# Kernel optimization log

Measured on AMD Instinct MI355X. Metric: run time of the kernel, lower is better.

The kernel has to match this reference:

```python
import jax, jax.numpy as jnp
import numpy as np

EPS = 1e-5      # BatchNorm1d default eps
K = 4           # branching factor of the ontology tree
HID = 6         # num_hiddens_genotype
LEVEL_SIZES = (64, 16, 4, 1)   # leaves -> root (term_layer_list order)
OFFSETS = (0, 64, 80, 84)      # slices into the stacked [85,...] term params


def setup_inputs() -> dict:
    key = jax.random.key(0)
    ks = jax.random.split(key, 8)
    B, G, GD, NT, NL = 4096, 4096, 24, 85, 64
    f32 = jnp.float32
    return {
        "x": jax.random.normal(ks[0], (B, G), f32),
        "gene_W": jax.random.normal(ks[1], (NL, GD, G), f32) * (1.0 / np.sqrt(G)),
        "gene_b": jnp.zeros((NL, GD), f32),
        "term_W": jax.random.normal(ks[2], (NT, HID, GD), f32) * (1.0 / np.sqrt(GD)),
        "term_b": jnp.zeros((NT, HID), f32),
        "bn_gamma": jnp.ones((NT, HID), f32),
        "bn_beta": jnp.zeros((NT, HID), f32),
        "aux1_W": jax.random.normal(ks[3], (NT, 1, HID), f32) * 0.1,
        "aux1_b": jnp.zeros((NT, 1), f32),
        "aux2_W": jax.random.normal(ks[4], (NT, 1, 1), f32) * 0.1,
        "aux2_b": jnp.zeros((NT, 1), f32),
        "final_W": jax.random.normal(ks[5], (HID, HID), f32) * (1.0 / np.sqrt(HID)),
        "final_b": jnp.zeros((HID,), f32),
        "fbn_gamma": jnp.ones((HID,), f32),
        "fbn_beta": jnp.zeros((HID,), f32),
        "faux_W": jax.random.normal(ks[6], (1, HID), f32) * 0.1,
        "faux_b": jnp.zeros((1,), f32),
        "fout_W": jax.random.normal(ks[7], (1, 1), f32) * 0.1,
        "fout_b": jnp.zeros((1,), f32),
    }


def _bn(z, g, b):
    # training-mode BatchNorm1d: batch mean / biased variance over axis 0
    mu = jnp.mean(z, axis=0, keepdims=True)
    var = jnp.mean((z - mu) ** 2, axis=0, keepdims=True)
    return (z - mu) * jax.lax.rsqrt(var + EPS) * g + b


def _forward(x, gene_W, gene_b, term_W, term_b, bn_gamma, bn_beta,
             aux1_W, aux1_b, aux2_W, aux2_b, final_W, final_b,
             fbn_gamma, fbn_beta, faux_W, faux_b, fout_W, fout_b):
    B = x.shape[0]
    # direct_gene_layers for all 64 leaf terms, batched: [B, 64, 24]
    h_in = jnp.einsum('bg,tkg->btk', x, gene_W) + gene_b
    aux_outs = []
    h = None
    for n, o in zip(LEVEL_SIZES, OFFSETS):  # leaves -> root (DAG topo order)
        if h is not None:
            # concat the K=4 children hidden states of each term: [B,n,K*HID]
            h_in = h.reshape(B, n, K * HID)
        # per-term Linear + tanh + BatchNorm, batched over the n terms
        z = jnp.tanh(jnp.einsum('bti,thi->bth', h_in, term_W[o:o + n]) + term_b[o:o + n])
        h = _bn(z, bn_gamma[o:o + n], bn_beta[o:o + n])  # [B, n, HID]
        # aux head: Linear(HID->1) -> tanh -> Linear(1->1)
        a1 = jnp.tanh(jnp.einsum('bth,toh->bto', h, aux1_W[o:o + n]) + aux1_b[o:o + n])
        a2 = a1 * aux2_W[o:o + n, 0] + aux2_b[o:o + n]   # [B, n, 1]
        aux_outs.append(a2[..., 0])
    root = h[:, 0, :]                                    # [B, HID]
    f = jnp.tanh(root @ final_W.T + final_b)
    mu = jnp.mean(f, axis=0)
    var = jnp.mean((f - mu) ** 2, axis=0)
    f = (f - mu) * jax.lax.rsqrt(var + EPS) * fbn_gamma + fbn_beta
    fa = jnp.tanh(f @ faux_W.T + faux_b)                 # [B, 1]
    pred = jax.nn.sigmoid(fa * fout_W[0, 0] + fout_b)    # [B, 1]
    # aux_out_map flattened in topo order, with 'final' prediction last: [B, 86]
    return jnp.concatenate(aux_outs + [pred], axis=1)


def reference(x, gene_W, gene_b, term_W, term_b, bn_gamma, bn_beta,
              aux1_W, aux1_b, aux2_W, aux2_b, final_W, final_b,
              fbn_gamma, fbn_beta, faux_W, faux_b, fout_W, fout_b):
    return _forward(x, gene_W, gene_b, term_W, term_b, bn_gamma, bn_beta,
                    aux1_W, aux1_b, aux2_W, aux2_b, final_W, final_b,
                    fbn_gamma, fbn_beta, faux_W, faux_b, fout_W, fout_b)
```

## Files before the change

### kernel.cpp

```cpp
#include <hip/hip_runtime.h>
#include <stdint.h>
#include <math.h>

#define EPSV   1e-5f
#define BATCH  4096
#define GDIM   4096
#define NF0    384
#define NSPLIT 8

typedef __attribute__((ext_vector_type(8))) short bf16x8;
typedef __attribute__((ext_vector_type(4))) float f32x4;
typedef __attribute__((ext_vector_type(2))) float f32x2;
typedef __attribute__((ext_vector_type(4))) uint32_t u32x4;

__device__ __forceinline__ uint32_t pkbf(float x, float y) {
    uint32_t a = __float_as_uint(x) + 0x8000u;
    uint32_t b = __float_as_uint(y) + 0x8000u;
    return __builtin_amdgcn_perm(b, a, 0x07060302u);
}
__device__ __forceinline__ uint16_t f2bf(float f) {
    return (uint16_t)((__float_as_uint(f) + 0x8000u) >> 16);
}
__device__ __forceinline__ float blo(uint32_t v) {
    union { uint32_t u; float f; } x; x.u = v << 16; return x.f;
}
__device__ __forceinline__ float bhi(uint32_t v) {
    union { uint32_t u; float f; } x; x.u = v & 0xffff0000u; return x.f;
}
__device__ __forceinline__ void glds16(const uint16_t* g, short* l) {
    __builtin_amdgcn_global_load_lds(
        (const __attribute__((address_space(1))) void*)g,
        (__attribute__((address_space(3))) void*)l, 16, 0, 0);
}

__global__ __launch_bounds__(256) void prep_kernel(
    const float* __restrict__ gene_W,
    const float* __restrict__ term_W, const float* __restrict__ term_b,
    const float* __restrict__ gene_b,
    uint16_t* __restrict__ m0, float* __restrict__ stats)
{
    const int tid = threadIdx.x;
    if (blockIdx.x == 0) {
        for (int j = tid; j < 1040; j += 256) stats[j] = 0.f;
        for (int f = tid; f < NF0; f += 256) {
            const int t = f / 6, h = f - t * 6;
            float b = term_b[f];
#pragma unroll
            for (int i = 0; i < 24; ++i)
                b += term_W[t * 144 + h * 24 + i] * gene_b[t * 24 + i];
            stats[1040 + f] = b;
        }
    }
    __shared__ float Wl[144];
    const int bid = blockIdx.x;
    const int t = bid >> 4;
    const int g = ((bid & 15) << 8) + tid;
    if (tid < 144) Wl[tid] = term_W[t * 144 + tid];
    __syncthreads();
    float gw[24];
#pragma unroll
    for (int i = 0; i < 24; ++i)
        gw[i] = gene_W[((size_t)t * 24 + i) * GDIM + g];
#pragma unroll
    for (int h = 0; h < 6; ++h) {
        float s = 0.f;
#pragma unroll
        for (int i = 0; i < 24; ++i) s += Wl[h * 24 + i] * gw[i];
        m0[((size_t)(t * 6 + h)) * GDIM + g] = f2bf(s);
    }
}

__global__ __launch_bounds__(512) void gemm_wide(
    const float* __restrict__ A32, const uint16_t* __restrict__ Bw,
    uint16_t* __restrict__ P, int KC)
{
    const int N = NF0, K = GDIM;
    __shared__ short sA[128 * 64];
    __shared__ short sB[2][384 * 64];
    const int tid  = threadIdx.x;
    const int m0   = blockIdx.x * 128;
    const int kbase = blockIdx.y * KC;
    uint16_t* Cp = P + (size_t)blockIdx.y * ((size_t)BATCH * NF0);
    const int wave = tid >> 6, lane = tid & 63;
    const int wm   = (wave >> 2) * 64;
    const int wn   = (wave & 3) * 96;
// ... 49 lines not shown
            for (int n = 0; n < 6; ++n)
                bfr[n] = *(const bf16x8*)&sB[cur][(wn + n * 16 + lm) * 64 + kk * 32 + quad * 8];
#pragma unroll
            for (int m = 0; m < 4; ++m)
#pragma unroll
                for (int n = 0; n < 6; ++n)
                    acc[m][n] = __builtin_amdgcn_mfma_f32_16x16x32_bf16(
                        af[m], bfr[n], acc[m][n], 0, 0, 0);
        }
        __builtin_amdgcn_s_barrier();
        a0 = n0v; a1 = n1v; a2 = n2v; a3 = n3v;
        cur ^= 1;
    }
    asm volatile("s_waitcnt vmcnt(0)" ::: "memory");
    {
        u32x4 pa0 = (u32x4){pkbf(a0[0],a0[1]), pkbf(a0[2],a0[3]),
                            pkbf(a1[0],a1[1]), pkbf(a1[2],a1[3])};
        u32x4 pa1 = (u32x4){pkbf(a2[0],a2[1]), pkbf(a2[2],a2[3]),
                            pkbf(a3[0],a3[1]), pkbf(a3[2],a3[3])};
        *(u32x4*)la = pa0;
        *(u32x4*)(la + 8) = pa1;
    }
    asm volatile("s_waitcnt lgkmcnt(0)" ::: "memory");
    __builtin_amdgcn_s_barrier();
#pragma unroll
    for (int kk = 0; kk < 2; ++kk) {
        bf16x8 af[4], bfr[6];
#pragma unroll
        for (int m = 0; m < 4; ++m)
            af[m]  = *(const bf16x8*)&sA[(wm + m * 16 + lm) * 64 + kk * 32 + quad * 8];
#pragma unroll
        for (int n = 0; n < 6; ++n)
            bfr[n] = *(const bf16x8*)&sB[cur][(wn + n * 16 + lm) * 64 + kk * 32 + quad * 8];
#pragma unroll
        for (int m = 0; m < 4; ++m)
#pragma unroll
            for (int n = 0; n < 6; ++n)
                acc[m][n] = __builtin_amdgcn_mfma_f32_16x16x32_bf16(
                    af[m], bfr[n], acc[m][n], 0, 0, 0);
    }
#pragma unroll
    for (int n = 0; n < 6; ++n) {
        const int col = wn + n * 16 + lm;
#pragma unroll
        for (int m = 0; m < 4; ++m) {
            const int row = m0 + wm + m * 16 + (quad << 2);
            uint16_t* cp = Cp + (size_t)row * N + col;
#pragma unroll
            for (int r = 0; r < 4; ++r) cp[(size_t)r * N] = f2bf(acc[m][n][r]);
        }
    }
}

__global__ __launch_bounds__(256) void lzero_kernel(
    const uint16_t* __restrict__ P, const float* __restrict__ bias0,
    float* __restrict__ z0, float* __restrict__ st0)
{
    __shared__ float red[4 * 768];
    const int tid  = threadIdx.x;
    const int lane = tid & 63, wave = tid >> 6;
    const uint32_t* P32 = (const uint32_t*)P;

    const f32x2 b0 = ((const f32x2*)bias0)[lane];
    const f32x2 b1 = ((const f32x2*)(bias0 + 128))[lane];
    const f32x2 b2 = ((const f32x2*)(bias0 + 256))[lane];

    float s[6], q[6];
#pragma unroll
    for (int k = 0; k < 6; ++k) { s[k] = 0.f; q[k] = 0.f; }

    const int rbase = blockIdx.x * 8 + wave * 2;
    for (int rl = 0; rl < 2; ++rl) {
        const int r = rbase + rl;
        float a0 = b0[0], a1 = b0[1], a2 = b1[0], a3 = b1[1], a4 = b2[0], a5 = b2[1];
        const uint32_t* pr = P32 + (size_t)r * 192 + lane;
#pragma unroll
        for (int z = 0; z < NSPLIT; ++z) {
            const uint32_t* p = pr + (size_t)z * ((size_t)BATCH * 192);
            uint32_t u0 = p[0], u1 = p[64], u2 = p[128];
            a0 += blo(u0); a1 += bhi(u0);
            a2 += blo(u1); a3 += bhi(u1);
            a4 += blo(u2); a5 += bhi(u2);
        }
        float z0v = tanhf(a0), z1v = tanhf(a1), z2v = tanhf(a2);
        float z3v = tanhf(a3), z4v = tanhf(a4), z5v = tanhf(a5);
        f32x2* zr = (f32x2*)(z0 + (size_t)r * NF0);
        zr[lane]       = (f32x2){z0v, z1v};
        zr[64 + lane]  = (f32x2){z2v, z3v};
        zr[128 + lane] = (f32x2){z4v, z5v};
        s[0] += z0v; q[0] += z0v * z0v;
        s[1] += z1v; q[1] += z1v * z1v;
        s[2] += z2v; q[2] += z2v * z2v;
        s[3] += z3v; q[3] += z3v * z3v;
        s[4] += z4v; q[4] += z4v * z4v;
        s[5] += z5v; q[5] += z5v * z5v;
    }
    float* rw = &red[wave * 768 + lane * 12];
#pragma unroll
    for (int k = 0; k < 6; ++k) { rw[k] = s[k]; rw[6 + k] = q[k]; }
    __syncthreads();
    for (int idx = tid; idx < 768; idx += 256) {
        float v = red[idx] + red[768 + idx] + red[1536 + idx] + red[2304 + idx];
        const int l = idx / 12, k = idx - l * 12;
        const int k6 = k % 6;
        const int f = (k6 >> 1) * 128 + 2 * l + (k6 & 1);
        atomicAdd(&st0[(k >= 6 ? NF0 : 0) + f], v);
    }
}

template <int N, int ROWS, int OFF, int PREV_OFF>
__global__ __launch_bounds__(256) void level_kernel(
    const float* __restrict__ in, float* __restrict__ z_out,
    const float* __restrict__ stats_prev, float* __restrict__ stats_out,
    const float* __restrict__ term_W, const float* __restrict__ term_b,
    const float* __restrict__ bn_gamma, const float* __restrict__ bn_beta,
    const float* __restrict__ aux1_W, const float* __restrict__ aux1_b,
    const float* __restrict__ aux2_W, const float* __restrict__ aux2_b,
    float* __restrict__ out)
{
    constexpr int IN_W  = 24 * N;
    constexpr int NFv   = 6 * N;
    constexpr int NG    = 256 / N;
    constexpr int ITERS = (ROWS * N) / 256;
    constexpr int NPREV = 4 * N;

    __shared__ float Wl[144 * N];
    __shared__ float tbl[6 * N];
    __shared__ float aA[IN_W];
    __shared__ float aC[IN_W];
    __shared__ float a1wL[6 * NPREV];
    __shared__ float a1bL[NPREV], a2wL[NPREV], a2bL[NPREV];
    __shared__ float ps[NG * NFv], pq[NG * NFv];

    const int tid = threadIdx.x;
    for (int idx = tid; idx < 144 * N; idx += 256) {
        int t = idx / 144, fh = idx - t * 144;
        Wl[fh * N + t] = term_W[(OFF + t) * 144 + fh];
    }
    for (int idx = tid; idx < 6 * N; idx += 256) {
        int t = idx / 6, h = idx - t * 6;
        tbl[h * N + t] = term_b[(OFF + t) * 6 + h];
    }
    {
        const float invB = 1.0f / BATCH;
        for (int j = tid; j < IN_W; j += 256) {
            float s = stats_prev[j], q = stats_prev[IN_W + j];
            float mu = s * invB;
            float var = q * invB - mu * mu;
            float rstd = rsqrtf(var + EPSV);
            float a = rstd * bn_gamma[PREV_OFF * 6 + j];
            int t = j / 24, i = j - t * 24;
            aA[i * N + t] = a;
            aC[i * N + t] = bn_beta[PREV_OFF * 6 + j] - mu * a;
        }
        for (int idx = tid; idx < 6 * NPREV; idx += 256) {
            int t = idx / 6, h = idx - t * 6;
            a1wL[h * NPREV + t] = aux1_W[(PREV_OFF + t) * 6 + h];
        }
        for (int t = tid; t < NPREV; t += 256) {
            a1bL[t] = aux1_b[PREV_OFF + t];
            a2wL[t] = aux2_W[PREV_OFF + t];
            a2bL[t] = aux2_b[PREV_OFF + t];
        }
    }
    __syncthreads();

    const int term = tid & (N - 1);
    const int grp  = tid / N;
    float s6[6], q6[6];
#pragma unroll
    for (int h = 0; h < 6; ++h) { s6[h] = 0.f; q6[h] = 0.f; }

    for (int it = 0; it < ITERS; ++it) {
        const int r = blockIdx.x * ROWS + it * NG + grp;
        const float* inrow = in + (size_t)r * IN_W + term * 24;
        float hv[24];
#pragma unroll
        for (int i4 = 0; i4 < 6; ++i4) {
            f32x4 v = *(const f32x4*)(inrow + 4 * i4);
            hv[4*i4+0] = v[0]; hv[4*i4+1] = v[1];
            hv[4*i4+2] = v[2]; hv[4*i4+3] = v[3];
        }
#pragma unroll
        for (int i = 0; i < 24; ++i)
            hv[i] = hv[i] * aA[i * N + term] + aC[i * N + term];
#pragma unroll
        for (int s = 0; s < 4; ++s) {
            const int tp = term * 4 + s;
            float acc = a1bL[tp];
#pragma unroll
            for (int h2 = 0; h2 < 6; ++h2) acc += hv[s * 6 + h2] * a1wL[h2 * NPREV + tp];
            float a1 = tanhf(acc);
            out[(size_t)r * 86 + PREV_OFF + tp] = a1 * a2wL[tp] + a2bL[tp];
        }
        float za[6];
#pragma unroll
        for (int h = 0; h < 6; ++h) za[h] = tbl[h * N + term];
#pragma unroll
        for (int i = 0; i < 24; ++i) {
            const float x = hv[i];
#pragma unroll
            for (int h = 0; h < 6; ++h) za[h] += x * Wl[(h * 24 + i) * N + term];
        }
        float* zr = z_out + (size_t)r * NFv + term * 6;
#pragma unroll
        for (int h = 0; h < 6; ++h) {
            float z = tanhf(za[h]);
            zr[h] = z;
            s6[h] += z;
            q6[h] += z * z;
        }
    }
#pragma unroll
    for (int h = 0; h < 6; ++h) {
        ps[grp * NFv + term * 6 + h] = s6[h];
        pq[grp * NFv + term * 6 + h] = q6[h];
    }
    __syncthreads();
    for (int f = tid; f < NFv; f += 256) {
        float s = 0.f, q = 0.f;
        for (int g2 = 0; g2 < NG; ++g2) { s += ps[g2 * NFv + f]; q += pq[g2 * NFv + f]; }
        atomicAdd(&stats_out[f], s);
        atomicAdd(&stats_out[NFv + f], q);
    }
}

__global__ __launch_bounds__(256) void final_p1(
    const float* __restrict__ z3, const float* __restrict__ st3,
    const float* __restrict__ bn_gamma, const float* __restrict__ bn_beta,
    const float* __restrict__ aux1_W, const float* __restrict__ aux1_b,
    const float* __restrict__ aux2_W, const float* __restrict__ aux2_b,
    const float* __restrict__ final_W, const float* __restrict__ final_b,
    float* __restrict__ fbuf, float* __restrict__ stf,
    float* __restrict__ out)
{
    __shared__ float wred[4][12];
    const int tid = threadIdx.x;
    const int r = blockIdx.x * 256 + tid;
    const float invB = 1.0f / BATCH;
    float a[6], c[6];
#pragma unroll
    for (int j = 0; j < 6; ++j) {
        float s = st3[j], q = st3[6 + j];
        float mu = s * invB, var = q * invB - mu * mu;
        float rstd = rsqrtf(var + EPSV);
        a[j] = rstd * bn_gamma[504 + j];
        c[j] = bn_beta[504 + j] - mu * a[j];
    }
    float h[6];
    {
        f32x2 z01 = *(const f32x2*)(z3 + (size_t)r * 6);
        f32x2 z23 = *(const f32x2*)(z3 + (size_t)r * 6 + 2);
        f32x2 z45 = *(const f32x2*)(z3 + (size_t)r * 6 + 4);
        h[0] = z01[0] * a[0] + c[0]; h[1] = z01[1] * a[1] + c[1];
        h[2] = z23[0] * a[2] + c[2]; h[3] = z23[1] * a[3] + c[3];
        h[4] = z45[0] * a[4] + c[4]; h[5] = z45[1] * a[5] + c[5];
    }
    float acc = aux1_b[84];
#pragma unroll
    for (int j = 0; j < 6; ++j) acc += h[j] * aux1_W[504 + j];
    out[(size_t)r * 86 + 84] = tanhf(acc) * aux2_W[84] + aux2_b[84];

    float f[6], s6[6], q6[6];
#pragma unroll
    for (int j = 0; j < 6; ++j) {
        float s = final_b[j];
#pragma unroll
        for (int k = 0; k < 6; ++k) s += h[k] * final_W[j * 6 + k];
        f[j] = tanhf(s);
        s6[j] = f[j]; q6[j] = f[j] * f[j];
    }
    {
        f32x2* fr = (f32x2*)(fbuf + (size_t)r * 6);
        fr[0] = (f32x2){f[0], f[1]};
        fr[1] = (f32x2){f[2], f[3]};
        fr[2] = (f32x2){f[4], f[5]};
    }
#pragma unroll
    for (int off = 32; off >= 1; off >>= 1) {
#pragma unroll
        for (int j = 0; j < 6; ++j) {
            s6[j] += __shfl_xor(s6[j], off, 64);
            q6[j] += __shfl_xor(q6[j], off, 64);
        }
    }
    const int wv = tid >> 6, ln = tid & 63;
    if (ln == 0) {
#pragma unroll
        for (int j = 0; j < 6; ++j) { wred[wv][j] = s6[j]; wred[wv][6 + j] = q6[j]; }
    }
    __syncthreads();
    if (tid < 12) {
        float s = wred[0][tid] + wred[1][tid] + wred[2][tid] + wred[3][tid];
        atomicAdd(&stf[tid], s);
    }
}

__global__ __launch_bounds__(256) void final_p2(
    const float* __restrict__ fbuf, const float* __restrict__ stf,
    const float* __restrict__ fbn_gamma, const float* __restrict__ fbn_beta,
    const float* __restrict__ faux_W, const float* __restrict__ faux_b,
    const float* __restrict__ fout_W, const float* __restrict__ fout_b,
    float* __restrict__ out)
{
    const int tid = threadIdx.x;
    const int r = blockIdx.x * 256 + tid;
    const float invB = 1.0f / BATCH;
    float av[6], cv[6];
#pragma unroll
    for (int j = 0; j < 6; ++j) {
        float mu = stf[j] * invB, var = stf[6 + j] * invB - mu * mu;
        float rstd = rsqrtf(var + EPSV);
        av[j] = rstd * fbn_gamma[j];
        cv[j] = fbn_beta[j] - mu * av[j];
    }
    float f[6];
    {
        f32x2 f01 = *(const f32x2*)(fbuf + (size_t)r * 6);
        f32x2 f23 = *(const f32x2*)(fbuf + (size_t)r * 6 + 2);
        f32x2 f45 = *(const f32x2*)(fbuf + (size_t)r * 6 + 4);
        f[0] = f01[0]; f[1] = f01[1]; f[2] = f23[0];
        f[3] = f23[1]; f[4] = f45[0]; f[5] = f45[1];
    }
    float acc2 = faux_b[0];
#pragma unroll
    for (int j = 0; j < 6; ++j) acc2 += (f[j] * av[j] + cv[j]) * faux_W[j];
    float fa  = tanhf(acc2);
    float pre = fa * fout_W[0] + fout_b[0];
    out[(size_t)r * 86 + 85] = 1.0f / (1.0f + expf(-pre));
}

extern "C" void kernel_launch(void* const* d_in, const int* in_sizes, int n_in,
                              void* d_out, int out_size, void* d_ws, size_t ws_size,
                              hipStream_t stream)
{
    const float* x      = (const float*)d_in[0];
    const float* gene_W = (const float*)d_in[1];
    const float* gene_b = (const float*)d_in[2];
    const float* term_W = (const float*)d_in[3];
    const float* term_b = (const float*)d_in[4];
    const float* bn_g   = (const float*)d_in[5];
    const float* bn_b   = (const float*)d_in[6];
    const float* a1W    = (const float*)d_in[7];
    const float* a1b    = (const float*)d_in[8];
    const float* a2W    = (const float*)d_in[9];
    const float* a2b    = (const float*)d_in[10];
    const float* fW     = (const float*)d_in[11];
    const float* fb     = (const float*)d_in[12];
    const float* fbn_g  = (const float*)d_in[13];
    const float* fbn_b  = (const float*)d_in[14];
    const float* fxW    = (const float*)d_in[15];
    const float* fxb    = (const float*)d_in[16];
    const float* foW    = (const float*)d_in[17];
    const float* fob    = (const float*)d_in[18];
    float* out = (float*)d_out;

    const size_t M0B = (size_t)NF0 * GDIM * 2;
    const size_t PB  = (size_t)NSPLIT * BATCH * NF0 * 2;
    const size_t Z0B = (size_t)BATCH * NF0 * 4;

    char* ws = (char*)d_ws;
    uint16_t* m0b  = (uint16_t*)ws;
    uint16_t* pbuf = (uint16_t*)(ws + M0B);
    float*    z0   = (float*)(ws + M0B + PB);
    float*    z1   = (float*)(ws + M0B + PB + Z0B);
    float*    z2   = (float*)(ws + M0B + PB + Z0B + 1572864);
    float*    z3   = (float*)(ws + M0B + PB + Z0B + 1572864 + 393216);
    float*    stats = (float*)(ws + M0B + PB + Z0B + 1572864 + 393216 + 98304);
    float* st0 = stats;
    float* st1 = stats + 768;
    float* st2 = stats + 960;
    float* st3 = stats + 1008;
    float* stf = stats + 1020;
    float* bias0 = stats + 1040;
    float* fbuf  = stats + 2048;

    prep_kernel<<<1024, 256, 0, stream>>>(gene_W, term_W, term_b, gene_b,
                                          m0b, stats);
    gemm_wide<<<dim3(32, NSPLIT), 512, 0, stream>>>(x, m0b, pbuf, GDIM / NSPLIT);
    lzero_kernel<<<512, 256, 0, stream>>>(pbuf, bias0, z0, st0);
    level_kernel<16, 16, 64, 0><<<256, 256, 0, stream>>>(
        z0, z1, st0, st1, term_W, term_b, bn_g, bn_b, a1W, a1b, a2W, a2b, out);
    level_kernel<4, 64, 80, 64><<<64, 256, 0, stream>>>(
        z1, z2, st1, st2, term_W, term_b, bn_g, bn_b, a1W, a1b, a2W, a2b, out);
    level_kernel<1, 256, 84, 80><<<16, 256, 0, stream>>>(
        z2, z3, st2, st3, term_W, term_b, bn_g, bn_b, a1W, a1b, a2W, a2b, out);
    final_p1<<<16, 256, 0, stream>>>(
        z3, st3, bn_g, bn_b, a1W, a1b, a2W, a2b, fW, fb, fbuf, stf, out);
    final_p2<<<16, 256, 0, stream>>>(
        fbuf, stf, fbn_g, fbn_b, fxW, fxb, foW, fob, out);
}
```

Baseline: 235.3 us.

## Fuse post-GEMM stages into one persistent kernel with grid barriers

Merges the level-zero reduction, the three tree-level kernels and both final-stage kernels into a single 256-block persistent kernel, with a software grid barrier (atomic counter plus generation flag) between stages. The goal is to remove per-launch overhead and the idle gaps between several small dependent kernels. In exchange, the level-zero stage runs on half as many blocks with more rows each. Most blocks sit idle at later barriers, and correctness depends on all 256 blocks being co-resident.

```diff
diff --git a/kernel.cpp b/kernel.cpp
--- a/kernel.cpp
+++ b/kernel.cpp
@@ -31,6 +31,30 @@
     __builtin_amdgcn_global_load_lds(
         (const __attribute__((address_space(1))) void*)g,
         (__attribute__((address_space(3))) void*)l, 16, 0, 0);
+}
+
+__device__ __forceinline__ void gbar(int* bar, int nblk) {
+    __syncthreads();
+    if (threadIdx.x == 0) {
+        __threadfence();
+        int gen = __hip_atomic_load(bar + 1, __ATOMIC_RELAXED,
+                                    __HIP_MEMORY_SCOPE_AGENT);
+        int prev = __hip_atomic_fetch_add(bar, 1, __ATOMIC_ACQ_REL,
+                                          __HIP_MEMORY_SCOPE_AGENT);
+        if (prev == nblk - 1) {
+            __hip_atomic_store(bar, 0, __ATOMIC_RELAXED,
+                               __HIP_MEMORY_SCOPE_AGENT);
+            __hip_atomic_store(bar + 1, gen + 1, __ATOMIC_RELEASE,
+                               __HIP_MEMORY_SCOPE_AGENT);
+        } else {
+            while (__hip_atomic_load(bar + 1, __ATOMIC_ACQUIRE,
+                                     __HIP_MEMORY_SCOPE_AGENT) == gen) {
+                __builtin_amdgcn_s_sleep(1);
+            }
+        }
+        __threadfence();
+    }
+    __syncthreads();
 }
 
 __global__ __launch_bounds__(256) void prep_kernel(
@@ -186,11 +210,9 @@
     }
 }
 
-__global__ __launch_bounds__(256) void lzero_kernel(
-    const uint16_t* __restrict__ P, const float* __restrict__ bias0,
-    float* __restrict__ z0, float* __restrict__ st0)
-{
-    __shared__ float red[4 * 768];
+__device__ void lzero_stage(float* red, int bid, const uint16_t* P,
+                            const float* bias0, float* z0, float* st0)
+{
     const int tid  = threadIdx.x;
     const int lane = tid & 63, wave = tid >> 6;
     const uint32_t* P32 = (const uint32_t*)P;
@@ -203,8 +225,8 @@
 #pragma unroll
     for (int k = 0; k < 6; ++k) { s[k] = 0.f; q[k] = 0.f; }
 
-    const int rbase = blockIdx.x * 8 + wave * 2;
-    for (int rl = 0; rl < 2; ++rl) {
+    const int rbase = bid * 16 + wave * 4;
+    for (int rl = 0; rl < 4; ++rl) {
         const int r = rbase + rl;
         float a0 = b0[0], a1 = b0[1], a2 = b1[0], a3 = b1[1], a4 = b2[0], a5 = b2[1];
         const uint32_t* pr = P32 + (size_t)r * 192 + lane;
@@ -243,14 +265,14 @@
 }
 
 template <int N, int ROWS, int OFF, int PREV_OFF>
-__global__ __launch_bounds__(256) void level_kernel(
-    const float* __restrict__ in, float* __restrict__ z_out,
-    const float* __restrict__ stats_prev, float* __restrict__ stats_out,
-    const float* __restrict__ term_W, const float* __restrict__ term_b,
-    const float* __restrict__ bn_gamma, const float* __restrict__ bn_beta,
-    const float* __restrict__ aux1_W, const float* __restrict__ aux1_b,
-    const float* __restrict__ aux2_W, const float* __restrict__ aux2_b,
-    float* __restrict__ out)
+__device__ void level_stage(float* smem, int bid,
+    const float* in, float* z_out,
+    const float* stats_prev, float* stats_out,
+    const float* term_W, const float* term_b,
+    const float* bn_gamma, const float* bn_beta,
+    const float* aux1_W, const float* aux1_b,
+    const float* aux2_W, const float* aux2_b,
+    float* out)
 {
     constexpr int IN_W  = 24 * N;
     constexpr int NFv   = 6 * N;
@@ -258,13 +280,16 @@
     constexpr int ITERS = (ROWS * N) / 256;
     constexpr int NPREV = 4 * N;
 
-    __shared__ float Wl[144 * N];
-    __shared__ float tbl[6 * N];
-    __shared__ float aA[IN_W];
-    __shared__ float aC[IN_W];
-    __shared__ float a1wL[6 * NPREV];
-    __shared__ float a1bL[NPREV], a2wL[NPREV], a2bL[NPREV];
-    __shared__ float ps[NG * NFv], pq[NG * NFv];
+    float* Wl   = smem;
+    float* tbl  = Wl + 144 * N;
+    float* aA   = tbl + 6 * N;
+    float* aC   = aA + IN_W;
+    float* a1wL = aC + IN_W;
+    float* a1bL = a1wL + 6 * NPREV;
+    float* a2wL = a1bL + NPREV;
+    float* a2bL = a2wL + NPREV;
+    float* ps   = a2bL + NPREV;
+    float* pq   = ps + 1536;
 
     const int tid = threadIdx.x;
     for (int idx = tid; idx < 144 * N; idx += 256) {
@@ -306,7 +331,7 @@
     for (int h = 0; h < 6; ++h) { s6[h] = 0.f; q6[h] = 0.f; }
 
     for (int it = 0; it < ITERS; ++it) {
-        const int r = blockIdx.x * ROWS + it * NG + grp;
+        const int r = bid * ROWS + it * NG + grp;
         const float* inrow = in + (size_t)r * IN_W + term * 24;
         float hv[24];
 #pragma unroll
@@ -359,18 +384,16 @@
     }
 }
 
-__global__ __launch_bounds__(256) void final_p1(
-    const float* __restrict__ z3, const float* __restrict__ st3,
-    const float* __restrict__ bn_gamma, const float* __restrict__ bn_beta,
-    const float* __restrict__ aux1_W, const float* __restrict__ aux1_b,
-    const float* __restrict__ aux2_W, const float* __restrict__ aux2_b,
-    const float* __restrict__ final_W, const float* __restrict__ final_b,
-    float* __restrict__ fbuf, float* __restrict__ stf,
-    float* __restrict__ out)
-{
-    __shared__ float wred[4][12];
+__device__ void fp1_stage(float* wred, int bid,
+    const float* z3, const float* st3,
+    const float* bn_gamma, const float* bn_beta,
+    const float* aux1_W, const float* aux1_b,
+    const float* aux2_W, const float* aux2_b,
+    const float* final_W, const float* final_b,
+    float* fbuf, float* stf, float* out)
+{
     const int tid = threadIdx.x;
-    const int r = blockIdx.x * 256 + tid;
+    const int r = bid * 256 + tid;
     const float invB = 1.0f / BATCH;
     float a[6], c[6];
 #pragma unroll
@@ -421,24 +444,24 @@
     const int wv = tid >> 6, ln = tid & 63;
     if (ln == 0) {
 #pragma unroll
-        for (int j = 0; j < 6; ++j) { wred[wv][j] = s6[j]; wred[wv][6 + j] = q6[j]; }
+        for (int j = 0; j < 6; ++j) { wred[wv * 12 + j] = s6[j]; wred[wv * 12 + 6 + j] = q6[j]; }
     }
     __syncthreads();
     if (tid < 12) {
-        float s = wred[0][tid] + wred[1][tid] + wred[2][tid] + wred[3][tid];
+        float s = wred[tid] + wred[12 + tid] + wred[24 + tid] + wred[36 + tid];
         atomicAdd(&stf[tid], s);
     }
 }
 
-__global__ __launch_bounds__(256) void final_p2(
-    const float* __restrict__ fbuf, const float* __restrict__ stf,
-    const float* __restrict__ fbn_gamma, const float* __restrict__ fbn_beta,
-    const float* __restrict__ faux_W, const float* __restrict__ faux_b,
-    const float* __restrict__ fout_W, const float* __restrict__ fout_b,
-    float* __restrict__ out)
+__device__ void fp2_stage(int bid,
+    const float* fbuf, const float* stf,
+    const float* fbn_gamma, const float* fbn_beta,
+    const float* faux_W, const float* faux_b,
+    const float* fout_W, const float* fout_b,
+    float* out)
 {
     const int tid = threadIdx.x;
-    const int r = blockIdx.x * 256 + tid;
+    const int r = bid * 256 + tid;
     const float invB = 1.0f / BATCH;
     float av[6], cv[6];
 #pragma unroll
@@ -462,6 +485,52 @@
     float fa  = tanhf(acc2);
     float pre = fa * fout_W[0] + fout_b[0];
     out[(size_t)r * 86 + 85] = 1.0f / (1.0f + expf(-pre));
+}
+
+__global__ __launch_bounds__(256) void tail_fused(
+    const uint16_t* __restrict__ P, float* __restrict__ stats,
+    float* __restrict__ z0, float* __restrict__ z1,
+    float* __restrict__ z2, float* __restrict__ z3,
+    float* __restrict__ fbuf,
+    const float* __restrict__ term_W, const float* __restrict__ term_b,
+    const float* __restrict__ bn_g, const float* __restrict__ bn_b,
+    const float* __restrict__ a1W, const float* __restrict__ a1b,
+    const float* __restrict__ a2W, const float* __restrict__ a2b,
+    const float* __restrict__ fW, const float* __restrict__ fb,
+    const float* __restrict__ fbn_g, const float* __restrict__ fbn_b,
+    const float* __restrict__ fxW, const float* __restrict__ fxb,
+    const float* __restrict__ foW, const float* __restrict__ fob,
+    float* __restrict__ out)
+{
+    __shared__ float smem[6816];
+    const int bid = blockIdx.x;
+    float* st0 = stats;
+    float* st1 = stats + 768;
+    float* st2 = stats + 960;
+    float* st3 = stats + 1008;
+    float* stf = stats + 1020;
+    int*   bar = (int*)(stats + 1032);
+    float* bias0 = stats + 1040;
+
+    lzero_stage(smem, bid, P, bias0, z0, st0);
+    gbar(bar, 256);
+    level_stage<16, 16, 64, 0>(smem, bid, z0, z1, st0, st1,
+        term_W, term_b, bn_g, bn_b, a1W, a1b, a2W, a2b, out);
+    gbar(bar, 256);
+    if (bid < 64)
+        level_stage<4, 64, 80, 64>(smem, bid, z1, z2, st1, st2,
+            term_W, term_b, bn_g, bn_b, a1W, a1b, a2W, a2b, out);
+    gbar(bar, 256);
+    if (bid < 16)
+        level_stage<1, 256, 84, 80>(smem, bid, z2, z3, st2, st3,
+            term_W, term_b, bn_g, bn_b, a1W, a1b, a2W, a2b, out);
+    gbar(bar, 256);
+    if (bid < 16)
+        fp1_stage(smem, bid, z3, st3, bn_g, bn_b, a1W, a1b, a2W, a2b,
+                  fW, fb, fbuf, stf, out);
+    gbar(bar, 256);
+    if (bid < 16)
+        fp2_stage(bid, fbuf, stf, fbn_g, fbn_b, fxW, fxb, foW, fob, out);
 }
 
 extern "C" void kernel_launch(void* const* d_in, const int* in_sizes, int n_in,
@@ -501,26 +570,13 @@
     float*    z2   = (float*)(ws + M0B + PB + Z0B + 1572864);
     float*    z3   = (float*)(ws + M0B + PB + Z0B + 1572864 + 393216);
     float*    stats = (float*)(ws + M0B + PB + Z0B + 1572864 + 393216 + 98304);
-    float* st0 = stats;
-    float* st1 = stats + 768;
-    float* st2 = stats + 960;
-    float* st3 = stats + 1008;
-    float* stf = stats + 1020;
-    float* bias0 = stats + 1040;
     float* fbuf  = stats + 2048;
 
     prep_kernel<<<1024, 256, 0, stream>>>(gene_W, term_W, term_b, gene_b,
                                           m0b, stats);
     gemm_wide<<<dim3(32, NSPLIT), 512, 0, stream>>>(x, m0b, pbuf, GDIM / NSPLIT);
-    lzero_kernel<<<512, 256, 0, stream>>>(pbuf, bias0, z0, st0);
-    level_kernel<16, 16, 64, 0><<<256, 256, 0, stream>>>(
-        z0, z1, st0, st1, term_W, term_b, bn_g, bn_b, a1W, a1b, a2W, a2b, out);
-    level_kernel<4, 64, 80, 64><<<64, 256, 0, stream>>>(
-        z1, z2, st1, st2, term_W, term_b, bn_g, bn_b, a1W, a1b, a2W, a2b, out);
-    level_kernel<1, 256, 84, 80><<<16, 256, 0, stream>>>(
-        z2, z3, st2, st3, term_W, term_b, bn_g, bn_b, a1W, a1b, a2W, a2b, out);
-    final_p1<<<16, 256, 0, stream>>>(
-        z3, st3, bn_g, bn_b, a1W, a1b, a2W, a2b, fW, fb, fbuf, stf, out);
-    final_p2<<<16, 256, 0, stream>>>(
-        fbuf, stf, fbn_g, fbn_b, fxW, fxb, foW, fob, out);
-}
+    tail_fused<<<256, 256, 0, stream>>>(
+        pbuf, stats, z0, z1, z2, z3, fbuf, term_W, term_b,
+        bn_g, bn_b, a1W, a1b, a2W, a2b, fW, fb,
+        fbn_g, fbn_b, fxW, fxb, foW, fob, out);
+}
```

Result: slower. 361.0 us (+53.4%).

## Fuse post-GEMM level and final kernels into one persistent kernel with grid barriers

Applied to the files above, without the earlier changes.

Replaces the six post-GEMM launches (split-K reduce, three level kernels, two final kernels) with a single 256-block kernel. Each block keeps its 16 batch rows in shared memory across all tree levels, and software grid barriers on an atomic counter order the BatchNorm statistics passes. This removes several launch gaps and the global round trips for the intermediate z buffers. It relies on all 256 blocks being co-resident, since the spin barrier would deadlock otherwise. It also needs the counter zeroed by prep_kernel; the counter sits inside the stats region that block 0 clears.

```diff
diff --git a/kernel.cpp b/kernel.cpp
--- a/kernel.cpp
+++ b/kernel.cpp
@@ -31,6 +31,22 @@
     __builtin_amdgcn_global_load_lds(
         (const __attribute__((address_space(1))) void*)g,
         (__attribute__((address_space(3))) void*)l, 16, 0, 0);
+}
+__device__ __forceinline__ float aload(float* p) {
+    return __hip_atomic_load(p, __ATOMIC_RELAXED, __HIP_MEMORY_SCOPE_AGENT);
+}
+__device__ __forceinline__ void gbar(int* cnt, int target) {
+    __syncthreads();
+    if (threadIdx.x == 0) {
+        asm volatile("s_waitcnt vmcnt(0) lgkmcnt(0)" ::: "memory");
+        __hip_atomic_fetch_add(cnt, 1, __ATOMIC_RELAXED,
+                               __HIP_MEMORY_SCOPE_AGENT);
+        while (__hip_atomic_load(cnt, __ATOMIC_RELAXED,
+                                 __HIP_MEMORY_SCOPE_AGENT) < target)
+            __builtin_amdgcn_s_sleep(8);
+    }
+    __syncthreads();
+    asm volatile("" ::: "memory");
 }
 
 __global__ __launch_bounds__(256) void prep_kernel(
@@ -186,282 +202,366 @@
     }
 }
 
-__global__ __launch_bounds__(256) void lzero_kernel(
-    const uint16_t* __restrict__ P, const float* __restrict__ bias0,
-    float* __restrict__ z0, float* __restrict__ st0)
-{
-    __shared__ float red[4 * 768];
-    const int tid  = threadIdx.x;
-    const int lane = tid & 63, wave = tid >> 6;
-    const uint32_t* P32 = (const uint32_t*)P;
-
-    const f32x2 b0 = ((const f32x2*)bias0)[lane];
-    const f32x2 b1 = ((const f32x2*)(bias0 + 128))[lane];
-    const f32x2 b2 = ((const f32x2*)(bias0 + 256))[lane];
-
-    float s[6], q[6];
-#pragma unroll
-    for (int k = 0; k < 6; ++k) { s[k] = 0.f; q[k] = 0.f; }
-
-    const int rbase = blockIdx.x * 8 + wave * 2;
-    for (int rl = 0; rl < 2; ++rl) {
-        const int r = rbase + rl;
-        float a0 = b0[0], a1 = b0[1], a2 = b1[0], a3 = b1[1], a4 = b2[0], a5 = b2[1];
-        const uint32_t* pr = P32 + (size_t)r * 192 + lane;
-#pragma unroll
-        for (int z = 0; z < NSPLIT; ++z) {
-            const uint32_t* p = pr + (size_t)z * ((size_t)BATCH * 192);
-            uint32_t u0 = p[0], u1 = p[64], u2 = p[128];
-            a0 += blo(u0); a1 += bhi(u0);
-            a2 += blo(u1); a3 += bhi(u1);
-            a4 += blo(u2); a5 += bhi(u2);
-        }
-        float z0v = tanhf(a0), z1v = tanhf(a1), z2v = tanhf(a2);
-        float z3v = tanhf(a3), z4v = tanhf(a4), z5v = tanhf(a5);
-        f32x2* zr = (f32x2*)(z0 + (size_t)r * NF0);
-        zr[lane]       = (f32x2){z0v, z1v};
-        zr[64 + lane]  = (f32x2){z2v, z3v};
-        zr[128 + lane] = (f32x2){z4v, z5v};
-        s[0] += z0v; q[0] += z0v * z0v;
-        s[1] += z1v; q[1] += z1v * z1v;
-        s[2] += z2v; q[2] += z2v * z2v;
-        s[3] += z3v; q[3] += z3v * z3v;
-        s[4] += z4v; q[4] += z4v * z4v;
-        s[5] += z5v; q[5] += z5v * z5v;
-    }
-    float* rw = &red[wave * 768 + lane * 12];
-#pragma unroll
-    for (int k = 0; k < 6; ++k) { rw[k] = s[k]; rw[6 + k] = q[k]; }
-    __syncthreads();
-    for (int idx = tid; idx < 768; idx += 256) {
-        float v = red[idx] + red[768 + idx] + red[1536 + idx] + red[2304 + idx];
-        const int l = idx / 12, k = idx - l * 12;
-        const int k6 = k % 6;
-        const int f = (k6 >> 1) * 128 + 2 * l + (k6 & 1);
-        atomicAdd(&st0[(k >= 6 ? NF0 : 0) + f], v);
-    }
-}
-
-template <int N, int ROWS, int OFF, int PREV_OFF>
-__global__ __launch_bounds__(256) void level_kernel(
-    const float* __restrict__ in, float* __restrict__ z_out,
-    const float* __restrict__ stats_prev, float* __restrict__ stats_out,
+__global__ __launch_bounds__(256) void tail_fused(
+    const uint16_t* __restrict__ P, float* __restrict__ stats,
     const float* __restrict__ term_W, const float* __restrict__ term_b,
-    const float* __restrict__ bn_gamma, const float* __restrict__ bn_beta,
-    const float* __restrict__ aux1_W, const float* __restrict__ aux1_b,
-    const float* __restrict__ aux2_W, const float* __restrict__ aux2_b,
+    const float* __restrict__ bn_g, const float* __restrict__ bn_b,
+    const float* __restrict__ a1W, const float* __restrict__ a1b,
+    const float* __restrict__ a2W, const float* __restrict__ a2b,
+    const float* __restrict__ fW, const float* __restrict__ fb,
+    const float* __restrict__ fbn_g, const float* __restrict__ fbn_b,
+    const float* __restrict__ fxW, const float* __restrict__ fxb,
+    const float* __restrict__ foW, const float* __restrict__ fob,
     float* __restrict__ out)
 {
-    constexpr int IN_W  = 24 * N;
-    constexpr int NFv   = 6 * N;
-    constexpr int NG    = 256 / N;
-    constexpr int ITERS = (ROWS * N) / 256;
-    constexpr int NPREV = 4 * N;
-
-    __shared__ float Wl[144 * N];
-    __shared__ float tbl[6 * N];
-    __shared__ float aA[IN_W];
-    __shared__ float aC[IN_W];
-    __shared__ float a1wL[6 * NPREV];
-    __shared__ float a1bL[NPREV], a2wL[NPREV], a2bL[NPREV];
-    __shared__ float ps[NG * NFv], pq[NG * NFv];
+    __shared__ float zb0[16 * 388];
+    __shared__ float zb1[16 * 100];
+    __shared__ float zb2[16 * 25];
+    __shared__ float zb3[16 * 6];
+    __shared__ float fL[16 * 6];
+    __shared__ float scratch[6816];
 
     const int tid = threadIdx.x;
-    for (int idx = tid; idx < 144 * N; idx += 256) {
-        int t = idx / 144, fh = idx - t * 144;
-        Wl[fh * N + t] = term_W[(OFF + t) * 144 + fh];
-    }
-    for (int idx = tid; idx < 6 * N; idx += 256) {
-        int t = idx / 6, h = idx - t * 6;
-        tbl[h * N + t] = term_b[(OFF + t) * 6 + h];
-    }
+    const int bid = blockIdx.x;
+    float* st0 = stats;
+    float* st1 = stats + 768;
+    float* st2 = stats + 960;
+    float* st3 = stats + 1008;
+    float* stf = stats + 1020;
+    int*   cnt = (int*)(stats + 1032);
+    const float* bias0 = stats + 1040;
+    const float invB = 1.0f / BATCH;
+
     {
-        const float invB = 1.0f / BATCH;
-        for (int j = tid; j < IN_W; j += 256) {
-            float s = stats_prev[j], q = stats_prev[IN_W + j];
-            float mu = s * invB;
-            float var = q * invB - mu * mu;
+        const int lane = tid & 63, wave = tid >> 6;
+        const uint32_t* P32 = (const uint32_t*)P;
+        const f32x2 b0 = ((const f32x2*)bias0)[lane];
+        const f32x2 b1 = ((const f32x2*)(bias0 + 128))[lane];
+        const f32x2 b2 = ((const f32x2*)(bias0 + 256))[lane];
+        float s[6], q[6];
+#pragma unroll
+        for (int k = 0; k < 6; ++k) { s[k] = 0.f; q[k] = 0.f; }
+        for (int rl = 0; rl < 4; ++rl) {
+            const int lr = wave * 4 + rl;
+            const size_t r = (size_t)bid * 16 + lr;
+            float a0 = b0[0], a1 = b0[1], a2 = b1[0], a3 = b1[1], a4 = b2[0], a5 = b2[1];
+            const uint32_t* pr = P32 + r * 192 + lane;
+#pragma unroll
+            for (int z = 0; z < NSPLIT; ++z) {
+                const uint32_t* p = pr + (size_t)z * ((size_t)BATCH * 192);
+                uint32_t u0 = p[0], u1 = p[64], u2 = p[128];
+                a0 += blo(u0); a1 += bhi(u0);
+                a2 += blo(u1); a3 += bhi(u1);
+                a4 += blo(u2); a5 += bhi(u2);
+            }
+            float z0v = tanhf(a0), z1v = tanhf(a1), z2v = tanhf(a2);
+            float z3v = tanhf(a3), z4v = tanhf(a4), z5v = tanhf(a5);
+            float* zr = &zb0[lr * 388];
+            zr[2 * lane]       = z0v; zr[2 * lane + 1]       = z1v;
+            zr[128 + 2 * lane] = z2v; zr[129 + 2 * lane]     = z3v;
+            zr[256 + 2 * lane] = z4v; zr[257 + 2 * lane]     = z5v;
+            s[0] += z0v; q[0] += z0v * z0v;
+            s[1] += z1v; q[1] += z1v * z1v;
+            s[2] += z2v; q[2] += z2v * z2v;
+            s[3] += z3v; q[3] += z3v * z3v;
+            s[4] += z4v; q[4] += z4v * z4v;
+            s[5] += z5v; q[5] += z5v * z5v;
+        }
+        float* rw = &scratch[wave * 768 + lane * 12];
+#pragma unroll
+        for (int k = 0; k < 6; ++k) { rw[k] = s[k]; rw[6 + k] = q[k]; }
+        __syncthreads();
+        for (int idx = tid; idx < 768; idx += 256) {
+            float v = scratch[idx] + scratch[768 + idx] +
+                      scratch[1536 + idx] + scratch[2304 + idx];
+            const int l = idx / 12, k = idx - l * 12;
+            const int k6 = k % 6;
+            const int f = (k6 >> 1) * 128 + 2 * l + (k6 & 1);
+            atomicAdd(&st0[(k >= 6 ? NF0 : 0) + f], v);
+        }
+    }
+    gbar(cnt, 256);
+
+    {
+        float* Wl  = scratch;
+        float* tbl = Wl + 2304;
+        float* aAs = tbl + 96;
+        float* aCs = aAs + 384;
+        float* w1  = aCs + 384;
+        float* b1v = w1 + 384;
+        float* w2  = b1v + 64;
+        float* b2v = w2 + 64;
+        float* ps  = b2v + 64;
+        float* pq  = ps + 1536;
+        for (int j = tid; j < 2304; j += 256) Wl[j] = term_W[64 * 144 + j];
+        for (int j = tid; j < 96; j += 256)   tbl[j] = term_b[64 * 6 + j];
+        for (int j = tid; j < 384; j += 256) {
+            float sv = aload(st0 + j), qv = aload(st0 + 384 + j);
+            float mu = sv * invB, var = qv * invB - mu * mu;
             float rstd = rsqrtf(var + EPSV);
-            float a = rstd * bn_gamma[PREV_OFF * 6 + j];
-            int t = j / 24, i = j - t * 24;
-            aA[i * N + t] = a;
-            aC[i * N + t] = bn_beta[PREV_OFF * 6 + j] - mu * a;
-        }
-        for (int idx = tid; idx < 6 * NPREV; idx += 256) {
-            int t = idx / 6, h = idx - t * 6;
-            a1wL[h * NPREV + t] = aux1_W[(PREV_OFF + t) * 6 + h];
-        }
-        for (int t = tid; t < NPREV; t += 256) {
-            a1bL[t] = aux1_b[PREV_OFF + t];
-            a2wL[t] = aux2_W[PREV_OFF + t];
-            a2bL[t] = aux2_b[PREV_OFF + t];
-        }
-    }
-    __syncthreads();
-
-    const int term = tid & (N - 1);
-    const int grp  = tid / N;
-    float s6[6], q6[6];
-#pragma unroll
-    for (int h = 0; h < 6; ++h) { s6[h] = 0.f; q6[h] = 0.f; }
-
-    for (int it = 0; it < ITERS; ++it) {
-        const int r = blockIdx.x * ROWS + it * NG + grp;
-        const float* inrow = in + (size_t)r * IN_W + term * 24;
+            float a = rstd * bn_g[j];
+            aAs[j] = a; aCs[j] = bn_b[j] - mu * a;
+        }
+        for (int j = tid; j < 384; j += 256) w1[j] = a1W[j];
+        for (int j = tid; j < 64; j += 256) {
+            b1v[j] = a1b[j]; w2[j] = a2W[j]; b2v[j] = a2b[j];
+        }
+        __syncthreads();
+        const int term = tid & 15, row = tid >> 4;
+        const size_t rg = (size_t)bid * 16 + row;
         float hv[24];
-#pragma unroll
-        for (int i4 = 0; i4 < 6; ++i4) {
-            f32x4 v = *(const f32x4*)(inrow + 4 * i4);
-            hv[4*i4+0] = v[0]; hv[4*i4+1] = v[1];
-            hv[4*i4+2] = v[2]; hv[4*i4+3] = v[3];
+        {
+            const float* ir = &zb0[row * 388 + term * 24];
+#pragma unroll
+            for (int i4 = 0; i4 < 6; ++i4) {
+                f32x4 v = *(const f32x4*)(ir + 4 * i4);
+                hv[4*i4+0] = v[0]; hv[4*i4+1] = v[1];
+                hv[4*i4+2] = v[2]; hv[4*i4+3] = v[3];
+            }
         }
 #pragma unroll
         for (int i = 0; i < 24; ++i)
-            hv[i] = hv[i] * aA[i * N + term] + aC[i * N + term];
+            hv[i] = hv[i] * aAs[term * 24 + i] + aCs[term * 24 + i];
 #pragma unroll
         for (int s = 0; s < 4; ++s) {
             const int tp = term * 4 + s;
-            float acc = a1bL[tp];
-#pragma unroll
-            for (int h2 = 0; h2 < 6; ++h2) acc += hv[s * 6 + h2] * a1wL[h2 * NPREV + tp];
-            float a1 = tanhf(acc);
-            out[(size_t)r * 86 + PREV_OFF + tp] = a1 * a2wL[tp] + a2bL[tp];
+            float acc = b1v[tp];
+#pragma unroll
+            for (int h2 = 0; h2 < 6; ++h2) acc += hv[s * 6 + h2] * w1[tp * 6 + h2];
+            out[rg * 86 + tp] = tanhf(acc) * w2[tp] + b2v[tp];
         }
         float za[6];
 #pragma unroll
-        for (int h = 0; h < 6; ++h) za[h] = tbl[h * N + term];
+        for (int h = 0; h < 6; ++h) za[h] = tbl[term * 6 + h];
 #pragma unroll
         for (int i = 0; i < 24; ++i) {
             const float x = hv[i];
 #pragma unroll
-            for (int h = 0; h < 6; ++h) za[h] += x * Wl[(h * 24 + i) * N + term];
-        }
-        float* zr = z_out + (size_t)r * NFv + term * 6;
+            for (int h = 0; h < 6; ++h) za[h] += x * Wl[term * 144 + h * 24 + i];
+        }
 #pragma unroll
         for (int h = 0; h < 6; ++h) {
             float z = tanhf(za[h]);
-            zr[h] = z;
-            s6[h] += z;
-            q6[h] += z * z;
-        }
-    }
-#pragma unroll
-    for (int h = 0; h < 6; ++h) {
-        ps[grp * NFv + term * 6 + h] = s6[h];
-        pq[grp * NFv + term * 6 + h] = q6[h];
-    }
-    __syncthreads();
-    for (int f = tid; f < NFv; f += 256) {
-        float s = 0.f, q = 0.f;
-        for (int g2 = 0; g2 < NG; ++g2) { s += ps[g2 * NFv + f]; q += pq[g2 * NFv + f]; }
-        atomicAdd(&stats_out[f], s);
-        atomicAdd(&stats_out[NFv + f], q);
-    }
-}
-
-__global__ __launch_bounds__(256) void final_p1(
-    const float* __restrict__ z3, const float* __restrict__ st3,
-    const float* __restrict__ bn_gamma, const float* __restrict__ bn_beta,
-    const float* __restrict__ aux1_W, const float* __restrict__ aux1_b,
-    const float* __restrict__ aux2_W, const float* __restrict__ aux2_b,
-    const float* __restrict__ final_W, const float* __restrict__ final_b,
-    float* __restrict__ fbuf, float* __restrict__ stf,
-    float* __restrict__ out)
-{
-    __shared__ float wred[4][12];
-    const int tid = threadIdx.x;
-    const int r = blockIdx.x * 256 + tid;
-    const float invB = 1.0f / BATCH;
-    float a[6], c[6];
-#pragma unroll
-    for (int j = 0; j < 6; ++j) {
-        float s = st3[j], q = st3[6 + j];
-        float mu = s * invB, var = q * invB - mu * mu;
-        float rstd = rsqrtf(var + EPSV);
-        a[j] = rstd * bn_gamma[504 + j];
-        c[j] = bn_beta[504 + j] - mu * a[j];
-    }
-    float h[6];
+            zb1[row * 100 + term * 6 + h] = z;
+            ps[row * 96 + term * 6 + h] = z;
+            pq[row * 96 + term * 6 + h] = z * z;
+        }
+        __syncthreads();
+        if (tid < 96) {
+            float sv = 0.f, qv = 0.f;
+#pragma unroll
+            for (int r2 = 0; r2 < 16; ++r2) {
+                sv += ps[r2 * 96 + tid]; qv += pq[r2 * 96 + tid];
+            }
+            atomicAdd(&st1[tid], sv);
+            atomicAdd(&st1[96 + tid], qv);
+        }
+    }
+    gbar(cnt, 512);
+
     {
-        f32x2 z01 = *(const f32x2*)(z3 + (size_t)r * 6);
-        f32x2 z23 = *(const f32x2*)(z3 + (size_t)r * 6 + 2);
-        f32x2 z45 = *(const f32x2*)(z3 + (size_t)r * 6 + 4);
-        h[0] = z01[0] * a[0] + c[0]; h[1] = z01[1] * a[1] + c[1];
-        h[2] = z23[0] * a[2] + c[2]; h[3] = z23[1] * a[3] + c[3];
-        h[4] = z45[0] * a[4] + c[4]; h[5] = z45[1] * a[5] + c[5];
-    }
-    float acc = aux1_b[84];
-#pragma unroll
-    for (int j = 0; j < 6; ++j) acc += h[j] * aux1_W[504 + j];
-    out[(size_t)r * 86 + 84] = tanhf(acc) * aux2_W[84] + aux2_b[84];
-
-    float f[6], s6[6], q6[6];
-#pragma unroll
-    for (int j = 0; j < 6; ++j) {
-        float s = final_b[j];
-#pragma unroll
-        for (int k = 0; k < 6; ++k) s += h[k] * final_W[j * 6 + k];
-        f[j] = tanhf(s);
-        s6[j] = f[j]; q6[j] = f[j] * f[j];
-    }
+        float* Wl  = scratch;
+        float* tbl = Wl + 576;
+        float* aAs = tbl + 24;
+        float* aCs = aAs + 96;
+        float* w1  = aCs + 96;
+        float* b1v = w1 + 96;
+        float* w2  = b1v + 16;
+        float* b2v = w2 + 16;
+        float* ps  = b2v + 16;
+        float* pq  = ps + 384;
+        for (int j = tid; j < 576; j += 256) Wl[j] = term_W[80 * 144 + j];
+        if (tid < 24) tbl[tid] = term_b[80 * 6 + tid];
+        for (int j = tid; j < 96; j += 256) {
+            float sv = aload(st1 + j), qv = aload(st1 + 96 + j);
+            float mu = sv * invB, var = qv * invB - mu * mu;
+            float rstd = rsqrtf(var + EPSV);
+            float a = rstd * bn_g[384 + j];
+            aAs[j] = a; aCs[j] = bn_b[384 + j] - mu * a;
+        }
+        for (int j = tid; j < 96; j += 256) w1[j] = a1W[384 + j];
+        if (tid < 16) {
+            b1v[tid] = a1b[64 + tid]; w2[tid] = a2W[64 + tid]; b2v[tid] = a2b[64 + tid];
+        }
+        __syncthreads();
+        if (tid < 64) {
+            const int term = tid & 3, row = tid >> 2;
+            const size_t rg = (size_t)bid * 16 + row;
+            float hv[24];
+#pragma unroll
+            for (int i = 0; i < 24; ++i) hv[i] = zb1[row * 100 + term * 24 + i];
+#pragma unroll
+            for (int i = 0; i < 24; ++i)
+                hv[i] = hv[i] * aAs[term * 24 + i] + aCs[term * 24 + i];
+#pragma unroll
+            for (int s = 0; s < 4; ++s) {
+                const int tp = term * 4 + s;
+                float acc = b1v[tp];
+#pragma unroll
+                for (int h2 = 0; h2 < 6; ++h2) acc += hv[s * 6 + h2] * w1[tp * 6 + h2];
+                out[rg * 86 + 64 + tp] = tanhf(acc) * w2[tp] + b2v[tp];
+            }
+            float za[6];
+#pragma unroll
+            for (int h = 0; h < 6; ++h) za[h] = tbl[term * 6 + h];
+#pragma unroll
+            for (int i = 0; i < 24; ++i) {
+                const float x = hv[i];
+#pragma unroll
+                for (int h = 0; h < 6; ++h) za[h] += x * Wl[term * 144 + h * 24 + i];
+            }
+#pragma unroll
+            for (int h = 0; h < 6; ++h) {
+                float z = tanhf(za[h]);
+                zb2[row * 25 + term * 6 + h] = z;
+                ps[row * 24 + term * 6 + h] = z;
+                pq[row * 24 + term * 6 + h] = z * z;
+            }
+        }
+        __syncthreads();
+        if (tid < 24) {
+            float sv = 0.f, qv = 0.f;
+#pragma unroll
+            for (int r2 = 0; r2 < 16; ++r2) {
+                sv += ps[r2 * 24 + tid]; qv += pq[r2 * 24 + tid];
+            }
+            atomicAdd(&st2[tid], sv);
+            atomicAdd(&st2[24 + tid], qv);
+        }
+    }
+    gbar(cnt, 768);
+
     {
-        f32x2* fr = (f32x2*)(fbuf + (size_t)r * 6);
-        fr[0] = (f32x2){f[0], f[1]};
-        fr[1] = (f32x2){f[2], f[3]};
-        fr[2] = (f32x2){f[4], f[5]};
-    }
-#pragma unroll
-    for (int off = 32; off >= 1; off >>= 1) {
+        float* Wl  = scratch;
+        float* tbl = Wl + 144;
+        float* aAs = tbl + 6;
+        float* aCs = aAs + 24;
+        float* w1  = aCs + 24;
+        float* b1v = w1 + 24;
+        float* w2  = b1v + 4;
+        float* b2v = w2 + 4;
+        float* ps  = b2v + 4;
+        float* pq  = ps + 96;
+        if (tid < 144) Wl[tid] = term_W[84 * 144 + tid];
+        if (tid < 6)   tbl[tid] = term_b[84 * 6 + tid];
+        if (tid < 24) {
+            float sv = aload(st2 + tid), qv = aload(st2 + 24 + tid);
+            float mu = sv * invB, var = qv * invB - mu * mu;
+            float rstd = rsqrtf(var + EPSV);
+            float a = rstd * bn_g[480 + tid];
+            aAs[tid] = a; aCs[tid] = bn_b[480 + tid] - mu * a;
+            w1[tid] = a1W[480 + tid];
+        }
+        if (tid < 4) {
+            b1v[tid] = a1b[80 + tid]; w2[tid] = a2W[80 + tid]; b2v[tid] = a2b[80 + tid];
+        }
+        __syncthreads();
+        if (tid < 16) {
+            const int row = tid;
+            const size_t rg = (size_t)bid * 16 + row;
+            float hv[24];
+#pragma unroll
+            for (int i = 0; i < 24; ++i)
+                hv[i] = zb2[row * 25 + i] * aAs[i] + aCs[i];
+#pragma unroll
+            for (int s = 0; s < 4; ++s) {
+                float acc = b1v[s];
+#pragma unroll
+                for (int h2 = 0; h2 < 6; ++h2) acc += hv[s * 6 + h2] * w1[s * 6 + h2];
+                out[rg * 86 + 80 + s] = tanhf(acc) * w2[s] + b2v[s];
+            }
+            float za[6];
+#pragma unroll
+            for (int h = 0; h < 6; ++h) za[h] = tbl[h];
+#pragma unroll
+            for (int i = 0; i < 24; ++i) {
+                const float x = hv[i];
+#pragma unroll
+                for (int h = 0; h < 6; ++h) za[h] += x * Wl[h * 24 + i];
+            }
+#pragma unroll
+            for (int h = 0; h < 6; ++h) {
+                float z = tanhf(za[h]);
+                zb3[row * 6 + h] = z;
+                ps[row * 6 + h] = z;
+                pq[row * 6 + h] = z * z;
+            }
+        }
+        __syncthreads();
+        if (tid < 6) {
+            float sv = 0.f, qv = 0.f;
+#pragma unroll
+            for (int r2 = 0; r2 < 16; ++r2) {
+                sv += ps[r2 * 6 + tid]; qv += pq[r2 * 6 + tid];
+            }
+            atomicAdd(&st3[tid], sv);
+            atomicAdd(&st3[6 + tid], qv);
+        }
+    }
+    gbar(cnt, 1024);
+
+    {
+        float* ps = scratch;
+        if (tid < 16) {
+            const int row = tid;
+            const size_t rg = (size_t)bid * 16 + row;
+            float a[6], c[6];
+#pragma unroll
+            for (int j = 0; j < 6; ++j) {
+                float sv = aload(st3 + j), qv = aload(st3 + 6 + j);
+                float mu = sv * invB, var = qv * invB - mu * mu;
+                float rstd = rsqrtf(var + EPSV);
+                a[j] = rstd * bn_g[504 + j];
+                c[j] = bn_b[504 + j] - mu * a[j];
+            }
+            float h[6];
+#pragma unroll
+            for (int j = 0; j < 6; ++j) h[j] = zb3[row * 6 + j] * a[j] + c[j];
+            float acc = a1b[84];
+#pragma unroll
+            for (int j = 0; j < 6; ++j) acc += h[j] * a1W[504 + j];
+            out[rg * 86 + 84] = tanhf(acc) * a2W[84] + a2b[84];
+#pragma unroll
+            for (int j = 0; j < 6; ++j) {
+                float s = fb[j];
+#pragma unroll
+                for (int k = 0; k < 6; ++k) s += h[k] * fW[j * 6 + k];
+                float f = tanhf(s);
+                fL[row * 6 + j] = f;
+                ps[row * 12 + j] = f;
+                ps[row * 12 + 6 + j] = f * f;
+            }
+        }
+        __syncthreads();
+        if (tid < 12) {
+            float sv = 0.f;
+#pragma unroll
+            for (int r2 = 0; r2 < 16; ++r2) sv += ps[r2 * 12 + tid];
+            atomicAdd(&stf[tid], sv);
+        }
+    }
+    gbar(cnt, 1280);
+
+    if (tid < 16) {
+        const int row = tid;
+        const size_t rg = (size_t)bid * 16 + row;
+        float av[6], cv[6];
 #pragma unroll
         for (int j = 0; j < 6; ++j) {
-            s6[j] += __shfl_xor(s6[j], off, 64);
-            q6[j] += __shfl_xor(q6[j], off, 64);
-        }
-    }
-    const int wv = tid >> 6, ln = tid & 63;
-    if (ln == 0) {
-#pragma unroll
-        for (int j = 0; j < 6; ++j) { wred[wv][j] = s6[j]; wred[wv][6 + j] = q6[j]; }
-    }
-    __syncthreads();
-    if (tid < 12) {
-        float s = wred[0][tid] + wred[1][tid] + wred[2][tid] + wred[3][tid];
-        atomicAdd(&stf[tid], s);
-    }
-}
-
-__global__ __launch_bounds__(256) void final_p2(
-    const float* __restrict__ fbuf, const float* __restrict__ stf,
-    const float* __restrict__ fbn_gamma, const float* __restrict__ fbn_beta,
-    const float* __restrict__ faux_W, const float* __restrict__ faux_b,
-    const float* __restrict__ fout_W, const float* __restrict__ fout_b,
-    float* __restrict__ out)
-{
-    const int tid = threadIdx.x;
-    const int r = blockIdx.x * 256 + tid;
-    const float invB = 1.0f / BATCH;
-    float av[6], cv[6];
-#pragma unroll
-    for (int j = 0; j < 6; ++j) {
-        float mu = stf[j] * invB, var = stf[6 + j] * invB - mu * mu;
-        float rstd = rsqrtf(var + EPSV);
-        av[j] = rstd * fbn_gamma[j];
-        cv[j] = fbn_beta[j] - mu * av[j];
-    }
-    float f[6];
-    {
-        f32x2 f01 = *(const f32x2*)(fbuf + (size_t)r * 6);
-        f32x2 f23 = *(const f32x2*)(fbuf + (size_t)r * 6 + 2);
-        f32x2 f45 = *(const f32x2*)(fbuf + (size_t)r * 6 + 4);
-        f[0] = f01[0]; f[1] = f01[1]; f[2] = f23[0];
-        f[3] = f23[1]; f[4] = f45[0]; f[5] = f45[1];
-    }
-    float acc2 = faux_b[0];
-#pragma unroll
-    for (int j = 0; j < 6; ++j) acc2 += (f[j] * av[j] + cv[j]) * faux_W[j];
-    float fa  = tanhf(acc2);
-    float pre = fa * fout_W[0] + fout_b[0];
-    out[(size_t)r * 86 + 85] = 1.0f / (1.0f + expf(-pre));
+            float mu = aload(stf + j) * invB;
+            float var = aload(stf + 6 + j) * invB - mu * mu;
+            float rstd = rsqrtf(var + EPSV);
+            av[j] = rstd * fbn_g[j];
+            cv[j] = fbn_b[j] - mu * av[j];
+        }
+        float acc2 = fxb[0];
+#pragma unroll
+        for (int j = 0; j < 6; ++j)
+            acc2 += (fL[row * 6 + j] * av[j] + cv[j]) * fxW[j];
+        float fa  = tanhf(acc2);
+        float pre = fa * foW[0] + fob[0];
+        out[rg * 86 + 85] = 1.0f / (1.0f + expf(-pre));
+    }
 }
 
 extern "C" void kernel_launch(void* const* d_in, const int* in_sizes, int n_in,
@@ -491,36 +591,16 @@
 
     const size_t M0B = (size_t)NF0 * GDIM * 2;
     const size_t PB  = (size_t)NSPLIT * BATCH * NF0 * 2;
-    const size_t Z0B = (size_t)BATCH * NF0 * 4;
 
     char* ws = (char*)d_ws;
     uint16_t* m0b  = (uint16_t*)ws;
     uint16_t* pbuf = (uint16_t*)(ws + M0B);
-    float*    z0   = (float*)(ws + M0B + PB);
-    float*    z1   = (float*)(ws + M0B + PB + Z0B);
-    float*    z2   = (float*)(ws + M0B + PB + Z0B + 1572864);
-    float*    z3   = (float*)(ws + M0B + PB + Z0B + 1572864 + 393216);
-    float*    stats = (float*)(ws + M0B + PB + Z0B + 1572864 + 393216 + 98304);
-    float* st0 = stats;
-    float* st1 = stats + 768;
-    float* st2 = stats + 960;
-    float* st3 = stats + 1008;
-    float* stf = stats + 1020;
-    float* bias0 = stats + 1040;
-    float* fbuf  = stats + 2048;
+    float*    stats = (float*)(ws + M0B + PB);
 
     prep_kernel<<<1024, 256, 0, stream>>>(gene_W, term_W, term_b, gene_b,
                                           m0b, stats);
     gemm_wide<<<dim3(32, NSPLIT), 512, 0, stream>>>(x, m0b, pbuf, GDIM / NSPLIT);
-    lzero_kernel<<<512, 256, 0, stream>>>(pbuf, bias0, z0, st0);
-    level_kernel<16, 16, 64, 0><<<256, 256, 0, stream>>>(
-        z0, z1, st0, st1, term_W, term_b, bn_g, bn_b, a1W, a1b, a2W, a2b, out);
-    level_kernel<4, 64, 80, 64><<<64, 256, 0, stream>>>(
-        z1, z2, st1, st2, term_W, term_b, bn_g, bn_b, a1W, a1b, a2W, a2b, out);
-    level_kernel<1, 256, 84, 80><<<16, 256, 0, stream>>>(
-        z2, z3, st2, st3, term_W, term_b, bn_g, bn_b, a1W, a1b, a2W, a2b, out);
-    final_p1<<<16, 256, 0, stream>>>(
-        z3, st3, bn_g, bn_b, a1W, a1b, a2W, a2b, fW, fb, fbuf, stf, out);
-    final_p2<<<16, 256, 0, stream>>>(
-        fbuf, stf, fbn_g, fbn_b, fxW, fxb, foW, fob, out);
-}
+    tail_fused<<<256, 256, 0, stream>>>(
+        pbuf, stats, term_W, term_b, bn_g, bn_b, a1W, a1b, a2W, a2b,
+        fW, fb, fbn_g, fbn_b, fxW, fxb, foW, fob, out);
+}
```

Result: slower. 249.6 us (+6.1%).
